# Kernel tuning notes

Measured on AMD Instinct MI355X. Metric: run time of the kernel, lower is better.

Reference implementation:

```python
import jax, jax.numpy as jnp
from jax import lax
import numpy as np

NEG = -1.0e9


def setup_inputs() -> dict:
    key = jax.random.key(0)
    k1, k2, k3 = jax.random.split(key, 3)
    B, N, W = 512, 8192, 15
    token_scores = jax.random.normal(k1, (B, N), dtype=jnp.float32)
    attention_mask = jax.random.randint(k2, (B, N), 0, 2).astype(jnp.int32)
    gamma = jnp.float32(1.0)
    width_logits = 0.1 * jax.random.normal(k3, (W,), dtype=jnp.float32)
    return {
        "token_scores": token_scores,
        "attention_mask": attention_mask,
        "gamma": gamma,
        "width_logits": width_logits,
    }


def _span_boost(masked, width_weights, max_span_width):
    # masked: [B, N] scores with padding set to NEG
    B, N = masked.shape
    boost = jnp.full((B, N), NEG, dtype=masked.dtype)
    for w in range(2, min(max_span_width + 1, N + 1)):
        # sliding min over windows of size w -> [B, N-w+1] (one per window start)
        span_mins = lax.reduce_window(
            masked, jnp.inf, lax.min,
            window_dimensions=(1, w), window_strides=(1, 1), padding="VALID")
        weighted = span_mins * width_weights[w - 2]
        # token p gets max over all window starts s with s <= p <= s+w-1:
        # sliding max with left/right pad (w-1) maps [B,N-w+1] back to [B,N]
        tok_boost = lax.reduce_window(
            weighted, -jnp.inf, lax.max,
            window_dimensions=(1, w), window_strides=(1, 1),
            padding=((0, 0), (w - 1, w - 1)))
        boost = jnp.maximum(boost, tok_boost)
    return boost


def reference(token_scores, attention_mask, gamma, width_logits):
    max_span_width = width_logits.shape[0]
    masked = jnp.where(attention_mask == 0, jnp.float32(NEG), token_scores)
    width_weights = jax.nn.softmax(width_logits, axis=0)
    boost = _span_boost(masked, width_weights, max_span_width)
    boost = jnp.maximum(boost, masked)
    return token_scores + gamma * boost
```

## Files before the change

kernel.cpp:

```cpp
#include <hip/hip_runtime.h>
#include <math.h>


constexpr float NEGV = -1.0e9f;
constexpr int W = 15;
constexpr int HALO = 14;
constexpr int CHUNK = 256;
constexpr int TILE = CHUNK + 2 * HALO;

__global__ __launch_bounds__(CHUNK)
void span_boost_kernel(const float* __restrict__ scores,
                       const int* __restrict__ mask,
                       const float* __restrict__ gamma_p,
                       const float* __restrict__ wlogits,
                       float* __restrict__ out,
                       int N, int chunksPerRow) {
    __shared__ float tile[TILE];
    __shared__ float wwS[W];

    const int tid = threadIdx.x;
    const int blk = blockIdx.x;
    const int row = blk / chunksPerRow;
    const int c0 = (blk - row * chunksPerRow) * CHUNK;
    const size_t rowOff = (size_t)row * (size_t)N;
    const float* srow = scores + rowOff;
    const int*   mrow = mask + rowOff;

    if (tid == 0) {
        float m = wlogits[0];
        #pragma unroll
        for (int i = 1; i < W; ++i) m = fmaxf(m, wlogits[i]);
        float e[W];
        float s = 0.f;
        #pragma unroll
        for (int i = 0; i < W; ++i) { e[i] = expf(wlogits[i] - m); s += e[i]; }
        const float inv = 1.0f / s;
        #pragma unroll
        for (int i = 0; i < W; ++i) wwS[i] = e[i] * inv;
    }

    #pragma unroll
    for (int l = tid; l < TILE; l += CHUNK) {
        const int g = c0 - HALO + l;
        float v = -INFINITY;
        if (g >= 0 && g < N) {
            const float sc = srow[g];
            const int   mk = mrow[g];
            v = (mk == 0) ? NEGV : sc;
        }
        tile[l] = v;
    }

    const int gp = c0 + tid;
    const float myScore = srow[gp];
    const float gamma = gamma_p[0];

    __syncthreads();

    float ww[HALO];
    #pragma unroll
    for (int i = 0; i < HALO; ++i)
        ww[i] = __int_as_float(__builtin_amdgcn_readfirstlane(__float_as_int(wwS[i])));

    const int li = HALO + tid;
    float cur = tile[li];
    const float myMasked = cur;
    float boost = -INFINITY;
    int la = li - 1;
    int ra = li + 1;

    #pragma unroll
    for (int t = 1; t <= HALO; ++t) {
        const float lv = tile[la];
        const float rv = tile[ra];
        const float pick = fmaxf(lv, rv);
        const bool goLeft = (lv >= rv);
        cur = fminf(cur, pick);
        boost = fmaxf(boost, cur * ww[t - 1]);
        la = goLeft ? la - 1 : la;
        ra = goLeft ? ra : ra + 1;
    }

    const float b = fmaxf(boost, myMasked);
    out[rowOff + gp] = myScore + gamma * b;
}

extern "C" void kernel_launch(void* const* d_in, const int* in_sizes, int n_in,
                              void* d_out, int out_size, void* d_ws, size_t ws_size,
                              hipStream_t stream) {
    const float* scores = (const float*)d_in[0];
    const int*   maskp  = (const int*)d_in[1];
    const float* gammap = (const float*)d_in[2];
    const float* wl     = (const float*)d_in[3];
    float* outp = (float*)d_out;

    const int N = 8192;
    const int B = in_sizes[0] / N;
    const int chunksPerRow = N / CHUNK;
    dim3 grid(B * chunksPerRow);
    span_boost_kernel<<<grid, CHUNK, 0, stream>>>(scores, maskp, gammap, wl, outp,
                                                  N, chunksPerRow);
}
```

Measured before the change: 106.4 us.

## Compute four tokens per thread with prefix-min split enumeration and float4 loads

Replaces the per-token greedy window expansion, a chain of data-dependent LDS reads, with a fixed-pattern computation. Each token now builds left and right prefix-min arrays from 36 register-cached tile values. For each span width it takes the max over all left/right splits of the min. Each thread handles four tokens, and global loads and stores use float4/int4, which cuts block count and relative halo overhead. In exchange it does O(W^2) min/max work per token and holds more registers.

```diff
diff --git a/kernel.cpp b/kernel.cpp
--- a/kernel.cpp
+++ b/kernel.cpp
@@ -4,34 +4,36 @@
 
 constexpr float NEGV = -1.0e9f;
 constexpr int W = 15;
-constexpr int HALO = 14;
-constexpr int CHUNK = 256;
-constexpr int TILE = CHUNK + 2 * HALO;
+constexpr int HALO = 16;
+constexpr int TPT = 4;
+constexpr int BLK = 256;
+constexpr int TOKS = BLK * TPT;
+constexpr int TILE_F = TOKS + 2 * HALO;
+constexpr int TILE_F4 = TILE_F / 4;
 
-__global__ __launch_bounds__(CHUNK)
+__global__ __launch_bounds__(BLK)
 void span_boost_kernel(const float* __restrict__ scores,
                        const int* __restrict__ mask,
                        const float* __restrict__ gamma_p,
                        const float* __restrict__ wlogits,
                        float* __restrict__ out,
                        int N, int chunksPerRow) {
-    __shared__ float tile[TILE];
+    __shared__ __align__(16) float tile[TILE_F];
     __shared__ float wwS[W];
 
     const int tid = threadIdx.x;
     const int blk = blockIdx.x;
     const int row = blk / chunksPerRow;
-    const int c0 = (blk - row * chunksPerRow) * CHUNK;
+    const int c0 = (blk - row * chunksPerRow) * TOKS;
     const size_t rowOff = (size_t)row * (size_t)N;
-    const float* srow = scores + rowOff;
-    const int*   mrow = mask + rowOff;
+    const float4* s4row = (const float4*)(scores + rowOff);
+    const int4*   m4row = (const int4*)(mask + rowOff);
 
     if (tid == 0) {
         float m = wlogits[0];
         #pragma unroll
         for (int i = 1; i < W; ++i) m = fmaxf(m, wlogits[i]);
-        float e[W];
-        float s = 0.f;
+        float e[W]; float s = 0.f;
         #pragma unroll
         for (int i = 0; i < W; ++i) { e[i] = expf(wlogits[i] - m); s += e[i]; }
         const float inv = 1.0f / s;
@@ -39,50 +41,68 @@
         for (int i = 0; i < W; ++i) wwS[i] = e[i] * inv;
     }
 
+    const int g4base = c0 / 4 - HALO / 4;
+    const int n4 = N / 4;
     #pragma unroll
-    for (int l = tid; l < TILE; l += CHUNK) {
-        const int g = c0 - HALO + l;
-        float v = -INFINITY;
-        if (g >= 0 && g < N) {
-            const float sc = srow[g];
-            const int   mk = mrow[g];
-            v = (mk == 0) ? NEGV : sc;
+    for (int l = tid; l < TILE_F4; l += BLK) {
+        const int g4 = g4base + l;
+        float4 v = make_float4(-INFINITY, -INFINITY, -INFINITY, -INFINITY);
+        if (g4 >= 0 && g4 < n4) {
+            const float4 sc = s4row[g4];
+            const int4   mk = m4row[g4];
+            v.x = (mk.x == 0) ? NEGV : sc.x;
+            v.y = (mk.y == 0) ? NEGV : sc.y;
+            v.z = (mk.z == 0) ? NEGV : sc.z;
+            v.w = (mk.w == 0) ? NEGV : sc.w;
         }
-        tile[l] = v;
+        ((float4*)tile)[l] = v;
     }
-
-    const int gp = c0 + tid;
-    const float myScore = srow[gp];
-    const float gamma = gamma_p[0];
 
     __syncthreads();
 
-    float ww[HALO];
+    float ww[W - 1];
     #pragma unroll
-    for (int i = 0; i < HALO; ++i)
+    for (int i = 0; i < W - 1; ++i)
         ww[i] = __int_as_float(__builtin_amdgcn_readfirstlane(__float_as_int(wwS[i])));
 
-    const int li = HALO + tid;
-    float cur = tile[li];
-    const float myMasked = cur;
-    float boost = -INFINITY;
-    int la = li - 1;
-    int ra = li + 1;
-
+    const int fb = tid * TPT;
+    float w[36];
     #pragma unroll
-    for (int t = 1; t <= HALO; ++t) {
-        const float lv = tile[la];
-        const float rv = tile[ra];
-        const float pick = fmaxf(lv, rv);
-        const bool goLeft = (lv >= rv);
-        cur = fminf(cur, pick);
-        boost = fmaxf(boost, cur * ww[t - 1]);
-        la = goLeft ? la - 1 : la;
-        ra = goLeft ? ra : ra + 1;
+    for (int q = 0; q < 9; ++q) {
+        const float4 v = *(const float4*)&tile[fb + 4 * q];
+        w[4 * q + 0] = v.x; w[4 * q + 1] = v.y; w[4 * q + 2] = v.z; w[4 * q + 3] = v.w;
     }
 
-    const float b = fmaxf(boost, myMasked);
-    out[rowOff + gp] = myScore + gamma * b;
+    const int gp4 = c0 / 4 + tid;
+    const float4 sc4 = s4row[gp4];
+    const float myScore[TPT] = { sc4.x, sc4.y, sc4.z, sc4.w };
+    const float gamma = gamma_p[0];
+
+    float res[TPT];
+    #pragma unroll
+    for (int r = 0; r < TPT; ++r) {
+        const float vp = w[16 + r];
+        float Ap[W], Bp[W];
+        Ap[0] = vp; Bp[0] = vp;
+        #pragma unroll
+        for (int j = 1; j < W; ++j) Ap[j] = fminf(Ap[j - 1], w[16 + r - j]);
+        #pragma unroll
+        for (int k = 1; k < W; ++k) Bp[k] = fminf(Bp[k - 1], w[16 + r + k]);
+
+        float boost = -INFINITY;
+        #pragma unroll
+        for (int t = 1; t <= W - 1; ++t) {
+            float d = fmaxf(Ap[t], Bp[t]);
+            #pragma unroll
+            for (int j = 1; j < t; ++j)
+                d = fmaxf(d, fminf(Ap[j], Bp[t - j]));
+            boost = fmaxf(boost, d * ww[t - 1]);
+        }
+        res[r] = myScore[r] + gamma * fmaxf(boost, vp);
+    }
+
+    float4 o4 = make_float4(res[0], res[1], res[2], res[3]);
+    ((float4*)(out + rowOff))[gp4] = o4;
 }
 
 extern "C" void kernel_launch(void* const* d_in, const int* in_sizes, int n_in,
@@ -96,8 +116,8 @@
 
     const int N = 8192;
     const int B = in_sizes[0] / N;
-    const int chunksPerRow = N / CHUNK;
+    const int chunksPerRow = N / TOKS;
     dim3 grid(B * chunksPerRow);
-    span_boost_kernel<<<grid, CHUNK, 0, stream>>>(scores, maskp, gammap, wl, outp,
-                                                  N, chunksPerRow);
+    span_boost_kernel<<<grid, BLK, 0, stream>>>(scores, maskp, gammap, wl, outp,
+                                                N, chunksPerRow);
 }
```

Result: no change. 106.9 us (+0.5%).
